# Performance work log

Measured on AMD Instinct MI355X. Metric: run time of the kernel, lower is better.

Reference implementation:

```python
import jax, jax.numpy as jnp
import numpy as np

D, H, N, BS = 3072, 2048, 16, 512
MAX_LATENT_VAR = 0.1


def setup_inputs() -> dict:
    key = jax.random.key(0)
    ks = jax.random.split(key, 12)
    s = 0.02
    return {
        "x": jax.random.normal(ks[0], (BS, D), dtype=jnp.float32),
        "eps": jax.random.normal(ks[1], (1, BS, N), dtype=jnp.float32),
        "enc_W1": jax.random.normal(ks[2], (D, H), dtype=jnp.float32) * s,
        "enc_b1": jnp.zeros((H,), dtype=jnp.float32),
        "enc_Wmu": jax.random.normal(ks[3], (H, N), dtype=jnp.float32) * s,
        "enc_bmu": jnp.zeros((N,), dtype=jnp.float32),
        "enc_Wls": jax.random.normal(ks[4], (H, 1), dtype=jnp.float32) * s,
        "enc_bls": jnp.zeros((1,), dtype=jnp.float32),
        "dec_W1": jax.random.normal(ks[5], (N, H), dtype=jnp.float32) * 0.1,
        "dec_b1": jnp.zeros((H,), dtype=jnp.float32),
        "dec_W2": jax.random.normal(ks[6], (H, D), dtype=jnp.float32) * s,
        "dec_b2": jnp.zeros((D,), dtype=jnp.float32),
    }


def reference(x, eps, enc_W1, enc_b1, enc_Wmu, enc_bmu, enc_Wls, enc_bls,
              dec_W1, dec_b1, dec_W2, dec_b2):
    bs, Dd = x.shape
    n = dec_W1.shape[0]

    def dec(z):  # smooth 2-layer MLP decoder (supports nested autodiff)
        return jnp.tanh(z @ dec_W1 + dec_b1) @ dec_W2 + dec_b2

    # encoder.forward_with_sigma
    h = jnp.tanh(x @ enc_W1 + enc_b1)
    z_star = h @ enc_Wmu + enc_bmu                      # (bs, n)
    sigma = jnp.exp(h @ enc_Wls + enc_bls)[:, 0]        # (bs,)

    # per-sample Jacobian of decoder: (bs, D, n)
    J = jax.vmap(jax.jacfwd(dec))(z_star)

    # per-sample Hessian of f(z) = stop_grad(d) . d,  d = (x - dec(z)) / sigma
    def f_hess(z, xi, sg):
        d = (xi - dec(z)) / sg
        return jnp.dot(jax.lax.stop_gradient(d), d)
    hess = jax.vmap(jax.hessian(f_hess), in_axes=(0, 0, 0))(z_star, x, sigma)  # (bs,n,n)

    eye = jnp.eye(n, dtype=x.dtype)
    Prec = jnp.einsum('bdi,bdj->bij', J, J) / (sigma ** 2)[:, None, None] + eye + hess

    eigvals = jnp.linalg.eigvalsh(Prec)                 # ascending, (bs, n)
    eigmin = eigvals[:, 0]
    delta = 1.0 / MAX_LATENT_VAR - eigmin               # (bs,)
    Prec = Prec + eye * delta[:, None, None]
    eigvals = eigvals + delta[:, None]

    # upper-triangular Cholesky: U^T U = Prec
    U = jnp.swapaxes(jnp.linalg.cholesky(Prec), -1, -2)  # (bs, n, n)

    def solve1(u, e):  # solve U y = e
        return jax.scipy.linalg.solve_triangular(u, e[:, None], lower=False)[:, 0]
    z_off = jax.vmap(jax.vmap(solve1, in_axes=(0, 0)), in_axes=(None, 0))(U, eps)  # (ne,bs,n)
    z_sample = z_star[None] + z_off

    n_eval = eps.shape[0]
    recon = dec(z_sample.reshape(-1, n)).reshape(n_eval, bs, Dd)
    recon_loss = ((recon - x[None]) ** 2).sum(axis=2).mean(axis=0) / (2.0 * sigma ** 2)
    latent_energy = (z_star ** 2).sum(axis=1) / 2.0 + (1.0 / eigvals).sum(axis=1) / 2.0
    logdet_loss = jnp.log(eigvals).sum(axis=1) / 2.0
    sigma_loss = Dd * jnp.log(sigma)
    neg_log_prob = (recon_loss + latent_energy + logdet_loss + sigma_loss) / Dd
    return (neg_log_prob, recon_loss, latent_energy, logdet_loss, sigma)
```

## Files before the change

### kernel.cpp

```cpp
#include <hip/hip_runtime.h>
#include <hip/hip_bf16.h>
#include <math.h>

#define D_ 3072
#define H_ 2048
#define N_ 16
#define BS_ 512
#define NSL_ 8

typedef short s16x8 __attribute__((ext_vector_type(8)));
typedef float f32x4v __attribute__((ext_vector_type(4)));
typedef __hip_bfloat16 bf16;

__device__ __forceinline__ void gload_lds16(const void* g, void* l) {
    __builtin_amdgcn_global_load_lds((const __attribute__((address_space(1))) void*)g,
                                     (__attribute__((address_space(3))) void*)l, 16, 0, 0);
}

__device__ __forceinline__ float bf2f(unsigned short u) {
    unsigned v = (unsigned)u << 16; float f; __builtin_memcpy(&f, &v, 4); return f;
}

__global__ __launch_bounds__(256) void mfma_nt_slab(
    const bf16* __restrict__ A, const bf16* __restrict__ Bt,
    float* __restrict__ C, int M, int N, int K, int KC)
{
    __shared__ __align__(16) bf16 As[128 * 32];
    __shared__ __align__(16) bf16 Bs[128 * 32];
    const int tid = threadIdx.x;
    const int w = tid >> 6, l = tid & 63;
    const int wr = w >> 1, wc = w & 1;
    const int m0 = blockIdx.y * 128, n0 = blockIdx.x * 128;
    const int kbeg = blockIdx.z * KC;
    float* Cz = C + (size_t)blockIdx.z * M * N;

    f32x4v acc[4][4];
    #pragma unroll
    for (int a = 0; a < 4; ++a)
        #pragma unroll
        for (int b = 0; b < 4; ++b) acc[a][b] = (f32x4v){0.f, 0.f, 0.f, 0.f};

    const int srow = l >> 2;
    const int scol = (l & 3) * 8;

    for (int k0 = kbeg; k0 < kbeg + KC; k0 += 32) {
        #pragma unroll
        for (int q = 0; q < 2; ++q) {
            int r0 = w * 32 + q * 16;
            gload_lds16(&A[(size_t)(m0 + r0 + srow) * K + k0 + scol], &As[r0 * 32]);
            gload_lds16(&Bt[(size_t)(n0 + r0 + srow) * K + k0 + scol], &Bs[r0 * 32]);
        }
        __syncthreads();
        s16x8 af[4], bfr[4];
        #pragma unroll
        for (int mf = 0; mf < 4; ++mf)
            af[mf] = *(const s16x8*)&As[(wr * 64 + mf * 16 + (l & 15)) * 32 + (l >> 4) * 8];
        #pragma unroll
        for (int nf = 0; nf < 4; ++nf)
            bfr[nf] = *(const s16x8*)&Bs[(wc * 64 + nf * 16 + (l & 15)) * 32 + (l >> 4) * 8];
        #pragma unroll
        for (int mf = 0; mf < 4; ++mf)
            #pragma unroll
            for (int nf = 0; nf < 4; ++nf)
                acc[mf][nf] = __builtin_amdgcn_mfma_f32_16x16x32_bf16(af[mf], bfr[nf], acc[mf][nf], 0, 0, 0);
        __syncthreads();
    }

    #pragma unroll
    for (int mf = 0; mf < 4; ++mf)
        #pragma unroll
        for (int nf = 0; nf < 4; ++nf) {
            int n = n0 + wc * 64 + nf * 16 + (l & 15);
            #pragma unroll
            for (int r = 0; r < 4; ++r) {
                int m = m0 + wr * 64 + mf * 16 + (l >> 4) * 4 + r;
                Cz[(size_t)m * N + n] = acc[mf][nf][r];
            }
        }
}

__global__ __launch_bounds__(256) void mfma_nt_sk(
    const bf16* __restrict__ A, const bf16* __restrict__ Bt,
    float* __restrict__ C, int M, int N, int K, int KC)
{
    __shared__ __align__(16) bf16 As[128 * 32];
    __shared__ __align__(16) bf16 Bs[128 * 32];
    const int tid = threadIdx.x;
    const int w = tid >> 6, l = tid & 63;
    const int wr = w >> 1, wc = w & 1;
    const int m0 = blockIdx.y * 128, n0 = blockIdx.x * 128;
    const int kbeg = blockIdx.z * KC;

    f32x4v acc[4][4];
    #pragma unroll
    for (int a = 0; a < 4; ++a)
        #pragma unroll
        for (int b = 0; b < 4; ++b) acc[a][b] = (f32x4v){0.f, 0.f, 0.f, 0.f};

    const int srow = l >> 2;
    const int scol = (l & 3) * 8;

    for (int k0 = kbeg; k0 < kbeg + KC; k0 += 32) {
        #pragma unroll
        for (int q = 0; q < 2; ++q) {
            int r0 = w * 32 + q * 16;
            gload_lds16(&A[(size_t)(m0 + r0 + srow) * K + k0 + scol], &As[r0 * 32]);
            gload_lds16(&Bt[(size_t)(n0 + r0 + srow) * K + k0 + scol], &Bs[r0 * 32]);
        }
        __syncthreads();
        s16x8 af[4], bfr[4];
        #pragma unroll
        for (int mf = 0; mf < 4; ++mf)
            af[mf] = *(const s16x8*)&As[(wr * 64 + mf * 16 + (l & 15)) * 32 + (l >> 4) * 8];
        #pragma unroll
        for (int nf = 0; nf < 4; ++nf)
            bfr[nf] = *(const s16x8*)&Bs[(wc * 64 + nf * 16 + (l & 15)) * 32 + (l >> 4) * 8];
        #pragma unroll
        for (int mf = 0; mf < 4; ++mf)
            #pragma unroll
            for (int nf = 0; nf < 4; ++nf)
                acc[mf][nf] = __builtin_amdgcn_mfma_f32_16x16x32_bf16(af[mf], bfr[nf], acc[mf][nf], 0, 0, 0);
        __syncthreads();
    }

    #pragma unroll
    for (int mf = 0; mf < 4; ++mf)
        #pragma unroll
        for (int nf = 0; nf < 4; ++nf) {
            int n = n0 + wc * 64 + nf * 16 + (l & 15);
            #pragma unroll
            for (int r = 0; r < 4; ++r) {
                int m = m0 + wr * 64 + mf * 16 + (l >> 4) * 4 + r;
                atomicAdd(&C[(size_t)m * N + n], acc[mf][nf][r]);
            }
        }
}

__global__ __launch_bounds__(256) void ep_ebf(const float* __restrict__ C8,
    const float* __restrict__ bias, const float* __restrict__ X,
    bf16* __restrict__ Eout, int MN, int N)
{
    const size_t SL = (size_t)MN;
    int base = (blockIdx.x * 256 + threadIdx.x) * 8;
    if (base < MN) {
        float v[8] = {0.f, 0.f, 0.f, 0.f, 0.f, 0.f, 0.f, 0.f};
        #pragma unroll
        for (int s = 0; s < NSL_; ++s) {
            float4 c0 = *(const float4*)&C8[s * SL + base];
            float4 c1 = *(const float4*)&C8[s * SL + base + 4];
            v[0] += c0.x; v[1] += c0.y; v[2] += c0.z; v[3] += c0.w;
            v[4] += c1.x; v[5] += c1.y; v[6] += c1.z; v[7] += c1.w;
        }
        float4 x0 = *(const float4*)&X[base];
        float4 x1 = *(const float4*)&X[base + 4];
        int n = base % N;
        float4 b0 = *(const float4*)&bias[n];
        float4 b1 = *(const float4*)&bias[n + 4];
        union { s16x8 vv; bf16 e[8]; } u;
        u.e[0] = __float2bfloat16(x0.x - (v[0] + b0.x));
        u.e[1] = __float2bfloat16(x0.y - (v[1] + b0.y));
        u.e[2] = __float2bfloat16(x0.z - (v[2] + b0.z));
        u.e[3] = __float2bfloat16(x0.w - (v[3] + b0.w));
        u.e[4] = __float2bfloat16(x1.x - (v[4] + b1.x));
        u.e[5] = __float2bfloat16(x1.y - (v[5] + b1.y));
        u.e[6] = __float2bfloat16(x1.z - (v[6] + b1.z));
        u.e[7] = __float2bfloat16(x1.w - (v[7] + b1.w));
        *(s16x8*)&Eout[base] = u.vv;
    }
}

__global__ __launch_bounds__(256) void ep_recon_fin(const float* __restrict__ C8,
    const float* __restrict__ bias, const float* __restrict__ X,
    const float* __restrict__ sigma, const float* __restrict__ lsig, float* __restrict__ d_out)
{
    const size_t SL = (size_t)BS_ * D_;
    int m = blockIdx.x;
    float s = 0.f;
    for (int n = threadIdx.x * 4; n < D_; n += 1024) {
        size_t i = (size_t)m * D_ + n;
        float4 acc4 = (float4){0.f, 0.f, 0.f, 0.f};
        #pragma unroll
        for (int sl = 0; sl < NSL_; ++sl) {
            float4 c = *(const float4*)&C8[sl * SL + i];
            acc4.x += c.x; acc4.y += c.y; acc4.z += c.z; acc4.w += c.w;
        }
        float4 bb = *(const float4*)&bias[n];
        float4 xx = *(const float4*)&X[i];
        float v0 = acc4.x + bb.x - xx.x;
        float v1 = acc4.y + bb.y - xx.y;
        float v2 = acc4.z + bb.z - xx.z;
        float v3 = acc4.w + bb.w - xx.w;
        s += v0 * v0 + v1 * v1 + v2 * v2 + v3 * v3;
    }
    __shared__ float red[4];
    int wid = threadIdx.x >> 6, lane = threadIdx.x & 63;
    #pragma unroll
    for (int off = 32; off; off >>= 1) s += __shfl_xor(s, off);
    if (lane == 0) red[wid] = s;
    __syncthreads();
    if (threadIdx.x == 0) {
        float tot = red[0] + red[1] + red[2] + red[3];
        float sg = sigma[m];
        float rl = tot / (2.0f * sg * sg);
        float le = d_out[2 * 512 + m];
        float ld = d_out[3 * 512 + m];
        d_out[m] = (rl + le + ld) / 3072.0f + lsig[m];
        d_out[512 + m] = rl;
    }
}

__global__ __launch_bounds__(256) void jtj_fused(
    const bf16* __restrict__ Vt, const bf16* __restrict__ W2t,
    float* __restrict__ S, int Mb, int b0)
{
    __shared__ union {
        struct { __align__(16) bf16 As[3][128 * 32]; __align__(16) bf16 Bs[3][128 * 32]; } s;
        __align__(16) bf16 J[128 * 136];
    } u;
    const int tid = threadIdx.x;
    const int w = tid >> 6, l = tid & 63;
    const int wr = w >> 1, wc = w & 1;

    int mb, nbk;
    if ((Mb & 7) == 0) {
        int lin = blockIdx.y * 24 + blockIdx.x;
        int xcd = lin & 7, idx = lin >> 3;
        int mchunk = Mb >> 3;
        mb = xcd * mchunk + idx / 24;
        nbk = idx % 24;
    } else { mb = blockIdx.y; nbk = blockIdx.x; }
    const int m0 = mb * 128, n0 = nbk * 128;

    f32x4v acc[4][4];
    #pragma unroll
    for (int a = 0; a < 4; ++a)
        #pragma unroll
        for (int b = 0; b < 4; ++b) acc[a][b] = (f32x4v){0.f, 0.f, 0.f, 0.f};

    const int strow = tid >> 2;
    const int scb = (((tid & 3) ^ ((tid >> 3) & 3)) << 4);

    auto STAGE = [&](int kt, int bi) {
        const char* a0 = (const char*)Vt  + ((size_t)(m0 + strow) * H_ + kt * 32) * 2 + scb;
        const char* b0p = (const char*)W2t + ((size_t)(n0 + strow) * H_ + kt * 32) * 2 + scb;
        char* la = (char*)u.s.As[bi] + w * 1024;
        char* lb = (char*)u.s.Bs[bi] + w * 1024;
        gload_lds16(a0, la);
        gload_lds16(a0 + (size_t)64 * H_ * 2, la + 4096);
        gload_lds16(b0p, lb);
        gload_lds16(b0p + (size_t)64 * H_ * 2, lb + 4096);
    };

    STAGE(0, 0);
    STAGE(1, 1);

    const int rdcb = (((l >> 4) ^ ((l >> 1) & 3)) << 4);

    for (int kt = 0; kt < H_ / 32; ++kt) {
        __builtin_amdgcn_sched_barrier(0);
        if (kt == H_ / 32 - 1) asm volatile("s_waitcnt vmcnt(0)" ::: "memory");
        else                   asm volatile("s_waitcnt vmcnt(4)" ::: "memory");
        __builtin_amdgcn_s_barrier();
        __builtin_amdgcn_sched_barrier(0);
        const int cur = kt % 3;
        const char* Ab = (const char*)u.s.As[cur];
        const char* Bb = (const char*)u.s.Bs[cur];
        s16x8 af[4], bfr[4];
        #pragma unroll
        for (int mf = 0; mf < 4; ++mf)
            af[mf] = *(const s16x8*)(Ab + (wr * 64 + mf * 16 + (l & 15)) * 64 + rdcb);
        #pragma unroll
        for (int nf = 0; nf < 4; ++nf)
            bfr[nf] = *(const s16x8*)(Bb + (wc * 64 + nf * 16 + (l & 15)) * 64 + rdcb);
        if (kt + 2 < H_ / 32) STAGE(kt + 2, (kt + 2) % 3);
        #pragma unroll
        for (int mf = 0; mf < 4; ++mf)
            #pragma unroll
            for (int nf = 0; nf < 4; ++nf)
                acc[mf][nf] = __builtin_amdgcn_mfma_f32_16x16x32_bf16(af[mf], bfr[nf], acc[mf][nf], 0, 0, 0);
    }

    __syncthreads();
    #pragma unroll
    for (int mf = 0; mf < 4; ++mf) {
        int rbase = wr * 64 + mf * 16 + (l >> 4) * 4;
        #pragma unroll
        for (int nf = 0; nf < 4; ++nf) {
            int col = wc * 64 + nf * 16 + (l & 15);
            #pragma unroll
            for (int r = 0; r < 4; ++r)
                u.J[(rbase + r) * 136 + col] = __float2bfloat16(acc[mf][nf][r]);
        }
    }
    __syncthreads();

    #pragma unroll
    for (int t2 = 0; t2 < 2; ++t2) {
        int bl = w * 2 + t2;
        f32x4v sp = (f32x4v){0.f, 0.f, 0.f, 0.f};
        #pragma unroll
        for (int kq = 0; kq < 4; ++kq) {
            s16x8 fr = *(const s16x8*)&u.J[(bl * 16 + (l & 15)) * 136 + kq * 32 + (l >> 4) * 8];
            sp = __builtin_amdgcn_mfma_f32_16x16x32_bf16(fr, fr, sp, 0, 0, 0);
        }
        int bglob = b0 + mb * 8 + bl;
        #pragma unroll
        for (int r = 0; r < 4; ++r)
            atomicAdd(&S[(size_t)bglob * 256 + ((l >> 4) * 4 + r) * 16 + (l & 15)], sp[r]);
    }
}

__global__ __launch_bounds__(256) void prep_all(
    const float* __restrict__ x, const float* __restrict__ enc_W1,
    const float* __restrict__ dec_W2, const float* __restrict__ dec_W1,
    bf16* __restrict__ x_bf, bf16* __restrict__ eW1t,
    bf16* __restrict__ W2t, bf16* __restrict__ W2b, bf16* __restrict__ W1b,
    float* __restrict__ zero_region)
{
    __shared__ float tile[64][65];
    const int blk = blockIdx.x;
    const int tid = threadIdx.x;
    if (blk < 768) {
        int i = blk * 256 + tid;
        const float4* p = (const float4*)x + (size_t)i * 2;
        float4 a = p[0], b = p[1];
        union { s16x8 v; bf16 e[8]; } u;
        u.e[0] = __float2bfloat16(a.x); u.e[1] = __float2bfloat16(a.y);
        u.e[2] = __float2bfloat16(a.z); u.e[3] = __float2bfloat16(a.w);
        u.e[4] = __float2bfloat16(b.x); u.e[5] = __float2bfloat16(b.y);
        u.e[6] = __float2bfloat16(b.z); u.e[7] = __float2bfloat16(b.w);
        *(s16x8*)&x_bf[(size_t)i * 8] = u.v;
    } else if (blk < 768 + 1536) {
        int bid = blk - 768;
        int r0 = (bid % 48) * 64, c0 = (bid / 48) * 64;
        int tx = tid & 63, ty = tid >> 6;
        #pragma unroll
        for (int k = 0; k < 16; ++k) {
            int rr = ty * 16 + k;
            tile[rr][tx] = enc_W1[(size_t)(r0 + rr) * H_ + c0 + tx];
        }
        __syncthreads();
        #pragma unroll
        for (int k = 0; k < 16; ++k) {
            int cc = ty * 16 + k;
            eW1t[(size_t)(c0 + cc) * D_ + r0 + tx] = __float2bfloat16(tile[tx][cc]);
        }
    } else if (blk < 768 + 3072) {
        int bid = blk - 768 - 1536;
        int r0 = (bid % 32) * 64, c0 = (bid / 32) * 64;
        int tx = tid & 63, ty = tid >> 6;
        #pragma unroll
        for (int k = 0; k < 16; ++k) {
            int rr = ty * 16 + k;
            float v = dec_W2[(size_t)(r0 + rr) * D_ + c0 + tx];
            tile[rr][tx] = v;
            W2b[(size_t)(r0 + rr) * D_ + c0 + tx] = __float2bfloat16(v);
        }
        __syncthreads();
        #pragma unroll
        for (int k = 0; k < 16; ++k) {
            int cc = ty * 16 + k;
            W2t[(size_t)(c0 + cc) * H_ + r0 + tx] = __float2bfloat16(tile[tx][cc]);
        }
    } else if (blk < 768 + 3072 + 16) {
        int i = (blk - 768 - 3072) * 256 + tid;
        if (i < N_ * H_ / 8) {
            const float4* p = (const float4*)dec_W1 + (size_t)i * 2;
            float4 a = p[0], b = p[1];
            union { s16x8 v; bf16 e[8]; } u;
            u.e[0] = __float2bfloat16(a.x); u.e[1] = __float2bfloat16(a.y);
            u.e[2] = __float2bfloat16(a.z); u.e[3] = __float2bfloat16(a.w);
            u.e[4] = __float2bfloat16(b.x); u.e[5] = __float2bfloat16(b.y);
            u.e[6] = __float2bfloat16(b.z); u.e[7] = __float2bfloat16(b.w);
            *(s16x8*)&W1b[(size_t)i * 8] = u.v;
        }
    } else {
        int i = (blk - 768 - 3072 - 16) * 256 + tid;
        *(float4*)&zero_region[(size_t)i * 4] = (float4){0.f, 0.f, 0.f, 0.f};
    }
}

__global__ __launch_bounds__(256) void zsig_t_kernel(const float* __restrict__ Ch8,
    const float* __restrict__ enc_b1, const float* __restrict__ Wmu, const float* __restrict__ bmu,
    const float* __restrict__ Wls, const float* __restrict__ bls,
    const float* __restrict__ dW1, const float* __restrict__ db1,
    float* __restrict__ z_star, float* __restrict__ lsig, float* __restrict__ sigma,
    float* __restrict__ t, bf16* __restrict__ tb, bf16* __restrict__ Vt)
{
    const int b = blockIdx.x, tid = threadIdx.x;
    const size_t SL = (size_t)BS_ * H_;
    float acc[17];
    #pragma unroll
    for (int i = 0; i < 17; ++i) acc[i] = 0.f;
    for (int hh = tid; hh < H_; hh += 256) {
        size_t idx = (size_t)b * H_ + hh;
        float c = 0.f;
        #pragma unroll
        for (int s = 0; s < NSL_; ++s) c += Ch8[s * SL + idx];
        float hv = tanhf(c + enc_b1[hh]);
        const float* wr = &Wmu[(size_t)hh * 16];
        #pragma unroll
        for (int i = 0; i < 16; ++i) acc[i] += hv * wr[i];
        acc[16] += hv * Wls[hh];
    }
    __shared__ float red[17][4];
    __shared__ float zs[16];
    __shared__ float us[H_];
    const int wid = tid >> 6, lane = tid & 63;
    #pragma unroll
    for (int i = 0; i < 17; ++i) {
        float v = acc[i];
        #pragma unroll
        for (int off = 32; off; off >>= 1) v += __shfl_xor(v, off);
        if (lane == 0) red[i][wid] = v;
    }
    __syncthreads();
    if (tid < 17) {
        float v = red[tid][0] + red[tid][1] + red[tid][2] + red[tid][3];
        if (tid < 16) { float z = v + bmu[tid]; zs[tid] = z; z_star[(size_t)b * 16 + tid] = z; }
        else { float ls = v + bls[0]; lsig[b] = ls; sigma[b] = expf(ls); }
    }
    __syncthreads();
    for (int hh = tid; hh < H_; hh += 256) {
        float a = db1[hh];
        #pragma unroll
        for (int i = 0; i < 16; ++i) a += zs[i] * dW1[(size_t)i * H_ + hh];
        float tv = tanhf(a);
        t[(size_t)b * H_ + hh] = tv;
        tb[(size_t)b * H_ + hh] = __float2bfloat16(tv);
        us[hh] = 1.f - tv * tv;
    }
    if (Vt) {
        __syncthreads();
        size_t base = (size_t)b * 16 * H_;
        int hh = tid * 8;
        for (int i = 0; i < 16; ++i) {
            union { s16x8 v; bf16 e[8]; } pk;
            #pragma unroll
            for (int k = 0; k < 8; ++k)
                pk.e[k] = __float2bfloat16(us[hh + k] * dW1[(size_t)i * H_ + hh + k]);
            *(s16x8*)&Vt[base + (size_t)i * H_ + hh] = pk.v;
        }
    }
}

__global__ __launch_bounds__(256) void build_t(const float* __restrict__ z,
    const float* __restrict__ W1, const float* __restrict__ b1, bf16* __restrict__ tb)
{
    __shared__ float zs[16];
    int b = blockIdx.x, tid = threadIdx.x;
    if (tid < 16) zs[tid] = z[(size_t)b * 16 + tid];
    __syncthreads();
    for (int hh = tid; hh < H_; hh += 256) {
        float a = b1[hh];
        #pragma unroll
        for (int i = 0; i < 16; ++i) a += zs[i] * W1[(size_t)i * H_ + hh];
        tb[(size_t)b * H_ + hh] = __float2bfloat16(tanhf(a));
    }
}

__global__ __launch_bounds__(256) void build_vt(const float* __restrict__ t,
    const float* __restrict__ W1, bf16* __restrict__ Vt, int b0)
{
    int bl = blockIdx.x, b = b0 + bl, tid = threadIdx.x;
    __shared__ float u[H_];
    for (int hh = tid; hh < H_; hh += 256) {
        float tv = t[(size_t)b * H_ + hh];
        u[hh] = 1.f - tv * tv;
    }
    __syncthreads();
    size_t base = (size_t)bl * 16 * H_;
    int hh = tid * 8;
    for (int i = 0; i < 16; ++i) {
        union { s16x8 v; bf16 e[8]; } pk;
        #pragma unroll
        for (int k = 0; k < 8; ++k)
            pk.e[k] = __float2bfloat16(u[hh + k] * W1[(size_t)i * H_ + hh + k]);
        *(s16x8*)&Vt[base + (size_t)i * H_ + hh] = pk.v;
    }
}

__global__ __launch_bounds__(256) void solve_hess_kernel(
    const float* __restrict__ S, const float* __restrict__ t, const float* __restrict__ g,
    const bf16* __restrict__ W1b, const float* __restrict__ sigma,
    const float* __restrict__ z_star, const float* __restrict__ eps,
    float* __restrict__ z_sample, float* __restrict__ d_out)
{
    __shared__ float Sh[4][256];
    const int tid = threadIdx.x;
    {
        const int w = tid >> 6, l = tid & 63;
        const int b = blockIdx.x * 4 + w;
        const int row = l & 15, kq = (l >> 4) * 8;
        f32x4v sp = (f32x4v){0.f, 0.f, 0.f, 0.f};
        for (int k0 = 0; k0 < H_; k0 += 32) {
            int kk = k0 + kq;
            s16x8 wf = *(const s16x8*)&W1b[(size_t)row * H_ + kk];
            float4 t0 = *(const float4*)&t[(size_t)b * H_ + kk];
            float4 t1 = *(const float4*)&t[(size_t)b * H_ + kk + 4];
            float4 g0 = *(const float4*)&g[(size_t)b * H_ + kk];
            float4 g1 = *(const float4*)&g[(size_t)b * H_ + kk + 4];
            float wv[8];
            wv[0] = 2.f * g0.x * t0.x * (1.f - t0.x * t0.x);
            wv[1] = 2.f * g0.y * t0.y * (1.f - t0.y * t0.y);
            wv[2] = 2.f * g0.z * t0.z * (1.f - t0.z * t0.z);
            wv[3] = 2.f * g0.w * t0.w * (1.f - t0.w * t0.w);
            wv[4] = 2.f * g1.x * t1.x * (1.f - t1.x * t1.x);
            wv[5] = 2.f * g1.y * t1.y * (1.f - t1.y * t1.y);
            wv[6] = 2.f * g1.z * t1.z * (1.f - t1.z * t1.z);
            wv[7] = 2.f * g1.w * t1.w * (1.f - t1.w * t1.w);
            union { s16x8 v; bf16 e[8]; } af;
            #pragma unroll
            for (int e = 0; e < 8; ++e)
                af.e[e] = __float2bfloat16(wv[e] * bf2f((unsigned short)wf[e]));
            sp = __builtin_amdgcn_mfma_f32_16x16x32_bf16(af.v, wf, sp, 0, 0, 0);
        }
        #pragma unroll
        for (int r = 0; r < 4; ++r)
            Sh[w][((l >> 4) * 4 + r) * 16 + (l & 15)] = sp[r];
    }
    __syncthreads();
    if (tid >= 64) return;

    const int lane = tid;
    const int q = lane >> 4;
    const int j = lane & 15;
    const int b = blockIdx.x * 4 + q;

    const float sg = sigma[b];
    const float inv_s2 = 1.0f / (sg * sg);

    float a0[16], a[16];
    #pragma unroll
    for (int r = 0; r < 16; ++r) {
        a0[r] = (S[(size_t)b * 256 + r * 16 + j] + Sh[q][r * 16 + j]) * inv_s2 + ((r == j) ? 1.0f : 0.0f);
        a[r] = a0[r];
    }

    #pragma unroll
    for (int k = 0; k < 14; ++k) {
        float x[16];
        #pragma unroll
        for (int r = 0; r < 16; ++r) x[r] = __shfl(a[k], r, 16);
        float sig2 = 0.f;
        #pragma unroll
        for (int r = 0; r < 16; ++r) if (r > k + 1) sig2 += x[r] * x[r];
        float x0 = x[k + 1];
        float normx = sqrtf(sig2 + x0 * x0);
        float alpha = (x0 >= 0.f) ? -normx : normx;
        float v[16];
        #pragma unroll
        for (int r = 0; r < 16; ++r)
            v[r] = (r <= k) ? 0.f : ((r == k + 1) ? x0 - alpha : x[r]);
        float vtv = 0.f;
        #pragma unroll
        for (int r = 0; r < 16; ++r) vtv += v[r] * v[r];
        float beta = (vtv > 1e-28f) ? 2.0f / vtv : 0.f;
        float sj = 0.f;
        #pragma unroll
        for (int r = 0; r < 16; ++r) sj += a[r] * v[r];
        float av[16];
        #pragma unroll
        for (int r = 0; r < 16; ++r) av[r] = __shfl(sj, r, 16);
        float vtav = 0.f;
        #pragma unroll
        for (int r = 0; r < 16; ++r) vtav += v[r] * av[r];
        float c = 0.5f * beta * vtav;
        float wv[16];
        #pragma unroll
        for (int r = 0; r < 16; ++r) wv[r] = beta * (av[r] - c * v[r]);
        float vj = (j <= k) ? 0.f : ((j == k + 1) ? a[k] - alpha : a[k]);
        float wj = beta * (sj - c * vj);
        #pragma unroll
        for (int r = 0; r < 16; ++r) a[r] -= v[r] * wj + wv[r] * vj;
    }

    float dg[16], eo[15];
    #pragma unroll
    for (int r = 0; r < 16; ++r) dg[r] = __shfl(a[r], r, 16);
    #pragma unroll
    for (int r = 0; r < 15; ++r) eo[r] = __shfl(a[r + 1], r, 16);

    float lo = 1e30f, hi = 1e30f;
    #pragma unroll
    for (int r = 0; r < 16; ++r) {
        float rad = ((r > 0) ? fabsf(eo[r - 1]) : 0.f) + ((r < 15) ? fabsf(eo[r]) : 0.f);
        lo = fminf(lo, dg[r] - rad);
        hi = fminf(hi, dg[r]);
    }
    lo -= 1e-4f; hi += 1e-4f;

    #pragma unroll
    for (int pass = 0; pass < 5; ++pass) {
        float step = (hi - lo) * (1.0f / 17.0f);
        float s = lo + step * (float)(j + 1);
        float qq = dg[0] - s;
        int cnt = (qq < 0.f) ? 1 : 0;
        #pragma unroll
        for (int i = 1; i < 16; ++i) {
            float denom = (fabsf(qq) < 1e-30f) ? -1e-30f : qq;
            qq = dg[i] - s - eo[i - 1] * eo[i - 1] / denom;
            cnt += (qq < 0.f) ? 1 : 0;
        }
        unsigned long long bal = __ballot(cnt >= 1);
        unsigned grp = (unsigned)((bal >> (q * 16)) & 0xffffull);
        int f = grp ? (__ffs(grp) - 1) : 16;
        float nlo = lo + step * (float)f;
        float nhi = (f < 16) ? (lo + step * (float)(f + 1)) : hi;
        lo = nlo; hi = nhi;
    }
    const float lam_min = 0.5f * (lo + hi);
    const float delta = 10.0f - lam_min;

    float bm[16];
    #pragma unroll
    for (int r = 0; r < 16; ++r) bm[r] = a0[r] + ((r == j) ? delta : 0.f);

    float ldsum = 0.f;
    #pragma unroll
    for (int kk = 0; kk < 16; ++kk) {
        float ck[16];
        #pragma unroll
        for (int r = 0; r < 16; ++r) ck[r] = __shfl(bm[kk], r, 16);
        float dkk = sqrtf(fmaxf(ck[kk], 1e-30f));
        float inv = 1.0f / dkk;
        ldsum += logf(dkk);
        float lfull[16];
        #pragma unroll
        for (int r = 0; r < 16; ++r) lfull[r] = ck[r] * inv;
        float lj = bm[kk] * inv;
        if (j == kk) {
            #pragma unroll
            for (int r = 0; r < 16; ++r) bm[r] = (r >= kk) ? lfull[r] : 0.f;
        } else if (j > kk) {
            #pragma unroll
            for (int r = 0; r < 16; ++r)
                if (r > kk) bm[r] -= lfull[r] * lj;
        }
    }

    float w[16];
    #pragma unroll
    for (int r = 0; r < 16; ++r) w[r] = 0.f;
    #pragma unroll
    for (int i = 0; i < 16; ++i) {
        float row[16];
        #pragma unroll
        for (int kx = 0; kx < 16; ++kx) row[kx] = __shfl(bm[i], kx, 16);
        float sacc = 0.f;
        #pragma unroll
        for (int kx = 0; kx < 16; ++kx) if (kx < i) sacc += row[kx] * w[kx];
        float invd = 1.0f / row[i];
        float val = (i == j) ? invd : (-sacc * invd);
        w[i] = (i >= j) ? val : 0.f;
    }

    float tsum = 0.f;
    #pragma unroll
    for (int r = 0; r < 16; ++r) tsum += w[r] * w[r];
    float zv = z_star[(size_t)b * 16 + j];
    float ep = eps[(size_t)b * 16 + j];
    float epsv[16];
    #pragma unroll
    for (int r = 0; r < 16; ++r) epsv[r] = __shfl(ep, r, 16);
    float zoff = 0.f;
    #pragma unroll
    for (int r = 0; r < 16; ++r) zoff += w[r] * epsv[r];
    z_sample[(size_t)b * 16 + j] = zv + zoff;

    float zsq = zv * zv;
    #pragma unroll
    for (int off = 1; off < 16; off <<= 1) {
        tsum += __shfl_xor(tsum, off);
        zsq  += __shfl_xor(zsq, off);
    }
    if (j == 0) {
        d_out[2 * 512 + b] = 0.5f * zsq + 0.5f * tsum;
        d_out[3 * 512 + b] = ldsum;
        d_out[4 * 512 + b] = sg;
    }
}

extern "C" void kernel_launch(void* const* d_in, const int* in_sizes, int n_in,
                              void* d_out, int out_size, void* d_ws, size_t ws_size,
                              hipStream_t stream)
{
    const float* x       = (const float*)d_in[0];
    const float* eps     = (const float*)d_in[1];
    const float* enc_W1  = (const float*)d_in[2];
    const float* enc_b1  = (const float*)d_in[3];
    const float* enc_Wmu = (const float*)d_in[4];
    const float* enc_bmu = (const float*)d_in[5];
    const float* enc_Wls = (const float*)d_in[6];
    const float* enc_bls = (const float*)d_in[7];
    const float* dec_W1  = (const float*)d_in[8];
    const float* dec_b1  = (const float*)d_in[9];
    const float* dec_W2  = (const float*)d_in[10];
    const float* dec_b2  = (const float*)d_in[11];
    float* out = (float*)d_out;

    char* wsb = (char*)d_ws;
    size_t off = 0;
    auto alloc = [&](size_t bytes) -> void* {
        off = (off + 255) & ~(size_t)255;
        void* p = wsb + off;
        off += bytes;
        return p;
    };

    float* g    = (float*)alloc((size_t)BS_ * H_ * 4);
    float* S    = (float*)alloc((size_t)BS_ * 256 * 4);

    float* Ch8  = (float*)alloc((size_t)NSL_ * BS_ * H_ * 4);
    float* Cd8  = (float*)alloc((size_t)NSL_ * BS_ * D_ * 4);
    float* t    = (float*)alloc((size_t)BS_ * H_ * 4);
    float* z_st = (float*)alloc((size_t)BS_ * 16 * 4);
    float* lsig = (float*)alloc(BS_ * 4);
    float* sigm = (float*)alloc(BS_ * 4);
    float* z_sm = (float*)alloc((size_t)BS_ * 16 * 4);
    bf16* x_bf  = (bf16*)alloc((size_t)BS_ * D_ * 2);
    bf16* eW1t  = (bf16*)alloc((size_t)H_ * D_ * 2);
    bf16* W2b   = (bf16*)alloc((size_t)H_ * D_ * 2);
    bf16* W2t   = (bf16*)alloc((size_t)D_ * H_ * 2);
    bf16* W1b   = (bf16*)alloc((size_t)N_ * H_ * 2);
    bf16* t_bf  = (bf16*)alloc((size_t)BS_ * H_ * 2);
    bf16* e_bf  = (bf16*)alloc((size_t)BS_ * D_ * 2);
    bf16* t2b   = (bf16*)alloc((size_t)BS_ * H_ * 2);

    int nb = 0;
    size_t base_off = off;
    const int cand[3] = {512, 128, 32};
    bf16* Vt = nullptr;
    for (int ci = 0; ci < 3; ++ci) {
        off = base_off;
        int n = cand[ci];
        bf16* vt = (bf16*)alloc((size_t)n * 16 * H_ * 2);
        if (off <= ws_size) { nb = n; Vt = vt; break; }
    }
    if (nb == 0) return;
    bf16* Vt_full = (nb == 512) ? Vt : nullptr;

    prep_all<<<dim3(768 + 3072 + 16 + 1152), 256, 0, stream>>>(
        x, enc_W1, dec_W2, dec_W1, x_bf, eW1t, W2t, W2b, W1b, g);

    mfma_nt_slab<<<dim3(H_ / 128, BS_ / 128, NSL_), 256, 0, stream>>>(
        x_bf, eW1t, Ch8, BS_, H_, D_, D_ / NSL_);
    zsig_t_kernel<<<dim3(BS_), 256, 0, stream>>>(Ch8, enc_b1, enc_Wmu, enc_bmu, enc_Wls, enc_bls,
        dec_W1, dec_b1, z_st, lsig, sigm, t, t_bf, Vt_full);
    mfma_nt_slab<<<dim3(D_ / 128, BS_ / 128, NSL_), 256, 0, stream>>>(
        t_bf, W2t, Cd8, BS_, D_, H_, H_ / NSL_);
    ep_ebf<<<dim3(BS_ * D_ / 8 / 256), 256, 0, stream>>>(Cd8, dec_b2, x, e_bf, BS_ * D_, D_);
    mfma_nt_sk<<<dim3(H_ / 128, BS_ / 128, 4), 256, 0, stream>>>(
        e_bf, W2b, g, BS_, H_, D_, D_ / 4);

    if (Vt_full) {
        jtj_fused<<<dim3(D_ / 128, 512 * 16 / 128), 256, 0, stream>>>(
            Vt_full, W2t, S, 512 * 16 / 128, 0);
    } else {
        for (int b0 = 0; b0 < BS_; b0 += nb) {
            build_vt<<<dim3(nb), 256, 0, stream>>>(t, dec_W1, Vt, b0);
            jtj_fused<<<dim3(D_ / 128, nb * 16 / 128), 256, 0, stream>>>(
                Vt, W2t, S, nb * 16 / 128, b0);
        }
    }

    solve_hess_kernel<<<dim3(BS_ / 4), 256, 0, stream>>>(
        S, t, g, W1b, sigm, z_st, eps, z_sm, out);
    build_t<<<dim3(BS_), 256, 0, stream>>>(z_sm, dec_W1, dec_b1, t2b);
    mfma_nt_slab<<<dim3(D_ / 128, BS_ / 128, NSL_), 256, 0, stream>>>(
        t2b, W2t, Cd8, BS_, D_, H_, H_ / NSL_);
    ep_recon_fin<<<dim3(BS_), 256, 0, stream>>>(Cd8, dec_b2, x, sigm, lsig, out);
}
```

Before: 310.6 us.

## Fuse decoder GEMM epilogue into JtJ launch and build_t into solve kernel

The first decoder GEMM (t·W2) is computed by 96 extra blocks inside the JtJ kernel launch, without split-K, writing the bf16 residual e directly. This removes the 8-slab fp32 atomic buffer, the ep_ebf reduction pass and a launch, and overlaps this GEMM with the JtJ work. The build_t step is folded into the end of solve_hess_kernel using z_sample held in shared memory, dropping another launch and a global round trip. The tradeoff is that each of the 96 e-blocks runs a full-K single-buffered loop that may become a tail, and the e_bf stores are scalar and uncoalesced.

```diff
diff --git a/kernel.cpp b/kernel.cpp
--- a/kernel.cpp
+++ b/kernel.cpp
@@ -136,39 +136,6 @@
         }
 }
 
-__global__ __launch_bounds__(256) void ep_ebf(const float* __restrict__ C8,
-    const float* __restrict__ bias, const float* __restrict__ X,
-    bf16* __restrict__ Eout, int MN, int N)
-{
-    const size_t SL = (size_t)MN;
-    int base = (blockIdx.x * 256 + threadIdx.x) * 8;
-    if (base < MN) {
-        float v[8] = {0.f, 0.f, 0.f, 0.f, 0.f, 0.f, 0.f, 0.f};
-        #pragma unroll
-        for (int s = 0; s < NSL_; ++s) {
-            float4 c0 = *(const float4*)&C8[s * SL + base];
-            float4 c1 = *(const float4*)&C8[s * SL + base + 4];
-            v[0] += c0.x; v[1] += c0.y; v[2] += c0.z; v[3] += c0.w;
-            v[4] += c1.x; v[5] += c1.y; v[6] += c1.z; v[7] += c1.w;
-        }
-        float4 x0 = *(const float4*)&X[base];
-        float4 x1 = *(const float4*)&X[base + 4];
-        int n = base % N;
-        float4 b0 = *(const float4*)&bias[n];
-        float4 b1 = *(const float4*)&bias[n + 4];
-        union { s16x8 vv; bf16 e[8]; } u;
-        u.e[0] = __float2bfloat16(x0.x - (v[0] + b0.x));
-        u.e[1] = __float2bfloat16(x0.y - (v[1] + b0.y));
-        u.e[2] = __float2bfloat16(x0.z - (v[2] + b0.z));
-        u.e[3] = __float2bfloat16(x0.w - (v[3] + b0.w));
-        u.e[4] = __float2bfloat16(x1.x - (v[4] + b1.x));
-        u.e[5] = __float2bfloat16(x1.y - (v[5] + b1.y));
-        u.e[6] = __float2bfloat16(x1.z - (v[6] + b1.z));
-        u.e[7] = __float2bfloat16(x1.w - (v[7] + b1.w));
-        *(s16x8*)&Eout[base] = u.vv;
-    }
-}
-
 __global__ __launch_bounds__(256) void ep_recon_fin(const float* __restrict__ C8,
     const float* __restrict__ bias, const float* __restrict__ X,
     const float* __restrict__ sigma, const float* __restrict__ lsig, float* __restrict__ d_out)
@@ -206,6 +173,157 @@
         float ld = d_out[3 * 512 + m];
         d_out[m] = (rl + le + ld) / 3072.0f + lsig[m];
         d_out[512 + m] = rl;
+    }
+}
+
+__global__ __launch_bounds__(256) void jtj_e_fused(
+    const bf16* __restrict__ Vt, const bf16* __restrict__ W2t,
+    float* __restrict__ S, int Mb,
+    const bf16* __restrict__ t_bf, const float* __restrict__ x,
+    const float* __restrict__ b2, bf16* __restrict__ e_bf)
+{
+    __shared__ union {
+        struct { __align__(16) bf16 As[3][128 * 32]; __align__(16) bf16 Bs[3][128 * 32]; } p;
+        __align__(16) bf16 J[128 * 136];
+        struct { __align__(16) bf16 As[128 * 32]; __align__(16) bf16 Bs[128 * 32]; } e;
+    } u;
+    const int tid = threadIdx.x;
+    const int w = tid >> 6, l = tid & 63;
+    const int wr = w >> 1, wc = w & 1;
+
+    if (blockIdx.x < 96) {
+        const int eb = blockIdx.x;
+        const int m0 = (eb / 24) * 128, n0 = (eb % 24) * 128;
+        f32x4v acc[4][4];
+        #pragma unroll
+        for (int a = 0; a < 4; ++a)
+            #pragma unroll
+            for (int b = 0; b < 4; ++b) acc[a][b] = (f32x4v){0.f, 0.f, 0.f, 0.f};
+        const int srow = l >> 2;
+        const int scol = (l & 3) * 8;
+        for (int k0 = 0; k0 < H_; k0 += 32) {
+            #pragma unroll
+            for (int q = 0; q < 2; ++q) {
+                int r0 = w * 32 + q * 16;
+                gload_lds16(&t_bf[(size_t)(m0 + r0 + srow) * H_ + k0 + scol], &u.e.As[r0 * 32]);
+                gload_lds16(&W2t[(size_t)(n0 + r0 + srow) * H_ + k0 + scol], &u.e.Bs[r0 * 32]);
+            }
+            __syncthreads();
+            s16x8 af[4], bfr[4];
+            #pragma unroll
+            for (int mf = 0; mf < 4; ++mf)
+                af[mf] = *(const s16x8*)&u.e.As[(wr * 64 + mf * 16 + (l & 15)) * 32 + (l >> 4) * 8];
+            #pragma unroll
+            for (int nf = 0; nf < 4; ++nf)
+                bfr[nf] = *(const s16x8*)&u.e.Bs[(wc * 64 + nf * 16 + (l & 15)) * 32 + (l >> 4) * 8];
+            #pragma unroll
+            for (int mf = 0; mf < 4; ++mf)
+                #pragma unroll
+                for (int nf = 0; nf < 4; ++nf)
+                    acc[mf][nf] = __builtin_amdgcn_mfma_f32_16x16x32_bf16(af[mf], bfr[nf], acc[mf][nf], 0, 0, 0);
+            __syncthreads();
+        }
+        #pragma unroll
+        for (int mf = 0; mf < 4; ++mf)
+            #pragma unroll
+            for (int nf = 0; nf < 4; ++nf) {
+                int n = n0 + wc * 64 + nf * 16 + (l & 15);
+                #pragma unroll
+                for (int r = 0; r < 4; ++r) {
+                    int m = m0 + wr * 64 + mf * 16 + (l >> 4) * 4 + r;
+                    size_t i = (size_t)m * D_ + n;
+                    e_bf[i] = __float2bfloat16(x[i] - (acc[mf][nf][r] + b2[n]));
+                }
+            }
+        return;
+    }
+
+    int lin = blockIdx.x - 96;
+    int mb, nbk;
+    if ((Mb & 7) == 0) {
+        int xcd = lin & 7, idx = lin >> 3;
+        int mchunk = Mb >> 3;
+        mb = xcd * mchunk + idx / 24;
+        nbk = idx % 24;
+    } else { mb = lin / 24; nbk = lin % 24; }
+    const int m0 = mb * 128, n0 = nbk * 128;
+
+    f32x4v acc[4][4];
+    #pragma unroll
+    for (int a = 0; a < 4; ++a)
+        #pragma unroll
+        for (int b = 0; b < 4; ++b) acc[a][b] = (f32x4v){0.f, 0.f, 0.f, 0.f};
+
+    const int strow = tid >> 2;
+    const int scb = (((tid & 3) ^ ((tid >> 3) & 3)) << 4);
+
+    auto STAGE = [&](int kt, int bi) {
+        const char* a0 = (const char*)Vt  + ((size_t)(m0 + strow) * H_ + kt * 32) * 2 + scb;
+        const char* b0p = (const char*)W2t + ((size_t)(n0 + strow) * H_ + kt * 32) * 2 + scb;
+        char* la = (char*)u.p.As[bi] + w * 1024;
+        char* lb = (char*)u.p.Bs[bi] + w * 1024;
+        gload_lds16(a0, la);
+        gload_lds16(a0 + (size_t)64 * H_ * 2, la + 4096);
+        gload_lds16(b0p, lb);
+        gload_lds16(b0p + (size_t)64 * H_ * 2, lb + 4096);
+    };
+
+    STAGE(0, 0);
+    STAGE(1, 1);
+
+    const int rdcb = (((l >> 4) ^ ((l >> 1) & 3)) << 4);
+
+    for (int kt = 0; kt < H_ / 32; ++kt) {
+        __builtin_amdgcn_sched_barrier(0);
+        if (kt == H_ / 32 - 1) asm volatile("s_waitcnt vmcnt(0)" ::: "memory");
+        else                   asm volatile("s_waitcnt vmcnt(4)" ::: "memory");
+        __builtin_amdgcn_s_barrier();
+        __builtin_amdgcn_sched_barrier(0);
+        const int cur = kt % 3;
+        const char* Ab = (const char*)u.p.As[cur];
+        const char* Bb = (const char*)u.p.Bs[cur];
+        s16x8 af[4], bfr[4];
+        #pragma unroll
+        for (int mf = 0; mf < 4; ++mf)
+            af[mf] = *(const s16x8*)(Ab + (wr * 64 + mf * 16 + (l & 15)) * 64 + rdcb);
+        #pragma unroll
+        for (int nf = 0; nf < 4; ++nf)
+            bfr[nf] = *(const s16x8*)(Bb + (wc * 64 + nf * 16 + (l & 15)) * 64 + rdcb);
+        if (kt + 2 < H_ / 32) STAGE(kt + 2, (kt + 2) % 3);
+        #pragma unroll
+        for (int mf = 0; mf < 4; ++mf)
+            #pragma unroll
+            for (int nf = 0; nf < 4; ++nf)
+                acc[mf][nf] = __builtin_amdgcn_mfma_f32_16x16x32_bf16(af[mf], bfr[nf], acc[mf][nf], 0, 0, 0);
+    }
+
+    __syncthreads();
+    #pragma unroll
+    for (int mf = 0; mf < 4; ++mf) {
+        int rbase = wr * 64 + mf * 16 + (l >> 4) * 4;
+        #pragma unroll
+        for (int nf = 0; nf < 4; ++nf) {
+            int col = wc * 64 + nf * 16 + (l & 15);
+            #pragma unroll
+            for (int r = 0; r < 4; ++r)
+                u.J[(rbase + r) * 136 + col] = __float2bfloat16(acc[mf][nf][r]);
+        }
+    }
+    __syncthreads();
+
+    #pragma unroll
+    for (int t2 = 0; t2 < 2; ++t2) {
+        int bl = w * 2 + t2;
+        f32x4v sp = (f32x4v){0.f, 0.f, 0.f, 0.f};
+        #pragma unroll
+        for (int kq = 0; kq < 4; ++kq) {
+            s16x8 fr = *(const s16x8*)&u.J[(bl * 16 + (l & 15)) * 136 + kq * 32 + (l >> 4) * 8];
+            sp = __builtin_amdgcn_mfma_f32_16x16x32_bf16(fr, fr, sp, 0, 0, 0);
+        }
+        int bglob = mb * 8 + bl;
+        #pragma unroll
+        for (int r = 0; r < 4; ++r)
+            atomicAdd(&S[(size_t)bglob * 256 + ((l >> 4) * 4 + r) * 16 + (l & 15)], sp[r]);
     }
 }
 
@@ -444,21 +562,6 @@
     }
 }
 
-__global__ __launch_bounds__(256) void build_t(const float* __restrict__ z,
-    const float* __restrict__ W1, const float* __restrict__ b1, bf16* __restrict__ tb)
-{
-    __shared__ float zs[16];
-    int b = blockIdx.x, tid = threadIdx.x;
-    if (tid < 16) zs[tid] = z[(size_t)b * 16 + tid];
-    __syncthreads();
-    for (int hh = tid; hh < H_; hh += 256) {
-        float a = b1[hh];
-        #pragma unroll
-        for (int i = 0; i < 16; ++i) a += zs[i] * W1[(size_t)i * H_ + hh];
-        tb[(size_t)b * H_ + hh] = __float2bfloat16(tanhf(a));
-    }
-}
-
 __global__ __launch_bounds__(256) void build_vt(const float* __restrict__ t,
     const float* __restrict__ W1, bf16* __restrict__ Vt, int b0)
 {
@@ -484,9 +587,11 @@
     const float* __restrict__ S, const float* __restrict__ t, const float* __restrict__ g,
     const bf16* __restrict__ W1b, const float* __restrict__ sigma,
     const float* __restrict__ z_star, const float* __restrict__ eps,
-    float* __restrict__ z_sample, float* __restrict__ d_out)
+    const float* __restrict__ dW1, const float* __restrict__ db1,
+    bf16* __restrict__ t2b, float* __restrict__ d_out)
 {
     __shared__ float Sh[4][256];
+    __shared__ float zs2[4][16];
     const int tid = threadIdx.x;
     {
         const int w = tid >> 6, l = tid & 63;
@@ -520,164 +625,177 @@
             Sh[w][((l >> 4) * 4 + r) * 16 + (l & 15)] = sp[r];
     }
     __syncthreads();
-    if (tid >= 64) return;
-
-    const int lane = tid;
-    const int q = lane >> 4;
-    const int j = lane & 15;
-    const int b = blockIdx.x * 4 + q;
-
-    const float sg = sigma[b];
-    const float inv_s2 = 1.0f / (sg * sg);
-
-    float a0[16], a[16];
-    #pragma unroll
-    for (int r = 0; r < 16; ++r) {
-        a0[r] = (S[(size_t)b * 256 + r * 16 + j] + Sh[q][r * 16 + j]) * inv_s2 + ((r == j) ? 1.0f : 0.0f);
-        a[r] = a0[r];
-    }
-
-    #pragma unroll
-    for (int k = 0; k < 14; ++k) {
-        float x[16];
-        #pragma unroll
-        for (int r = 0; r < 16; ++r) x[r] = __shfl(a[k], r, 16);
-        float sig2 = 0.f;
-        #pragma unroll
-        for (int r = 0; r < 16; ++r) if (r > k + 1) sig2 += x[r] * x[r];
-        float x0 = x[k + 1];
-        float normx = sqrtf(sig2 + x0 * x0);
-        float alpha = (x0 >= 0.f) ? -normx : normx;
-        float v[16];
-        #pragma unroll
-        for (int r = 0; r < 16; ++r)
-            v[r] = (r <= k) ? 0.f : ((r == k + 1) ? x0 - alpha : x[r]);
-        float vtv = 0.f;
-        #pragma unroll
-        for (int r = 0; r < 16; ++r) vtv += v[r] * v[r];
-        float beta = (vtv > 1e-28f) ? 2.0f / vtv : 0.f;
-        float sj = 0.f;
-        #pragma unroll
-        for (int r = 0; r < 16; ++r) sj += a[r] * v[r];
-        float av[16];
-        #pragma unroll
-        for (int r = 0; r < 16; ++r) av[r] = __shfl(sj, r, 16);
-        float vtav = 0.f;
-        #pragma unroll
-        for (int r = 0; r < 16; ++r) vtav += v[r] * av[r];
-        float c = 0.5f * beta * vtav;
-        float wv[16];
-        #pragma unroll
-        for (int r = 0; r < 16; ++r) wv[r] = beta * (av[r] - c * v[r]);
-        float vj = (j <= k) ? 0.f : ((j == k + 1) ? a[k] - alpha : a[k]);
-        float wj = beta * (sj - c * vj);
-        #pragma unroll
-        for (int r = 0; r < 16; ++r) a[r] -= v[r] * wj + wv[r] * vj;
-    }
-
-    float dg[16], eo[15];
-    #pragma unroll
-    for (int r = 0; r < 16; ++r) dg[r] = __shfl(a[r], r, 16);
-    #pragma unroll
-    for (int r = 0; r < 15; ++r) eo[r] = __shfl(a[r + 1], r, 16);
-
-    float lo = 1e30f, hi = 1e30f;
-    #pragma unroll
-    for (int r = 0; r < 16; ++r) {
-        float rad = ((r > 0) ? fabsf(eo[r - 1]) : 0.f) + ((r < 15) ? fabsf(eo[r]) : 0.f);
-        lo = fminf(lo, dg[r] - rad);
-        hi = fminf(hi, dg[r]);
-    }
-    lo -= 1e-4f; hi += 1e-4f;
-
-    #pragma unroll
-    for (int pass = 0; pass < 5; ++pass) {
-        float step = (hi - lo) * (1.0f / 17.0f);
-        float s = lo + step * (float)(j + 1);
-        float qq = dg[0] - s;
-        int cnt = (qq < 0.f) ? 1 : 0;
-        #pragma unroll
-        for (int i = 1; i < 16; ++i) {
-            float denom = (fabsf(qq) < 1e-30f) ? -1e-30f : qq;
-            qq = dg[i] - s - eo[i - 1] * eo[i - 1] / denom;
-            cnt += (qq < 0.f) ? 1 : 0;
-        }
-        unsigned long long bal = __ballot(cnt >= 1);
-        unsigned grp = (unsigned)((bal >> (q * 16)) & 0xffffull);
-        int f = grp ? (__ffs(grp) - 1) : 16;
-        float nlo = lo + step * (float)f;
-        float nhi = (f < 16) ? (lo + step * (float)(f + 1)) : hi;
-        lo = nlo; hi = nhi;
-    }
-    const float lam_min = 0.5f * (lo + hi);
-    const float delta = 10.0f - lam_min;
-
-    float bm[16];
-    #pragma unroll
-    for (int r = 0; r < 16; ++r) bm[r] = a0[r] + ((r == j) ? delta : 0.f);
-
-    float ldsum = 0.f;
-    #pragma unroll
-    for (int kk = 0; kk < 16; ++kk) {
-        float ck[16];
-        #pragma unroll
-        for (int r = 0; r < 16; ++r) ck[r] = __shfl(bm[kk], r, 16);
-        float dkk = sqrtf(fmaxf(ck[kk], 1e-30f));
-        float inv = 1.0f / dkk;
-        ldsum += logf(dkk);
-        float lfull[16];
-        #pragma unroll
-        for (int r = 0; r < 16; ++r) lfull[r] = ck[r] * inv;
-        float lj = bm[kk] * inv;
-        if (j == kk) {
-            #pragma unroll
-            for (int r = 0; r < 16; ++r) bm[r] = (r >= kk) ? lfull[r] : 0.f;
-        } else if (j > kk) {
+
+    if (tid < 64) {
+        const int lane = tid;
+        const int q = lane >> 4;
+        const int j = lane & 15;
+        const int b = blockIdx.x * 4 + q;
+
+        const float sg = sigma[b];
+        const float inv_s2 = 1.0f / (sg * sg);
+
+        float a0[16], a[16];
+        #pragma unroll
+        for (int r = 0; r < 16; ++r) {
+            a0[r] = (S[(size_t)b * 256 + r * 16 + j] + Sh[q][r * 16 + j]) * inv_s2 + ((r == j) ? 1.0f : 0.0f);
+            a[r] = a0[r];
+        }
+
+        #pragma unroll
+        for (int k = 0; k < 14; ++k) {
+            float x[16];
+            #pragma unroll
+            for (int r = 0; r < 16; ++r) x[r] = __shfl(a[k], r, 16);
+            float sig2 = 0.f;
+            #pragma unroll
+            for (int r = 0; r < 16; ++r) if (r > k + 1) sig2 += x[r] * x[r];
+            float x0 = x[k + 1];
+            float normx = sqrtf(sig2 + x0 * x0);
+            float alpha = (x0 >= 0.f) ? -normx : normx;
+            float v[16];
             #pragma unroll
             for (int r = 0; r < 16; ++r)
-                if (r > kk) bm[r] -= lfull[r] * lj;
-        }
-    }
-
-    float w[16];
-    #pragma unroll
-    for (int r = 0; r < 16; ++r) w[r] = 0.f;
-    #pragma unroll
-    for (int i = 0; i < 16; ++i) {
-        float row[16];
-        #pragma unroll
-        for (int kx = 0; kx < 16; ++kx) row[kx] = __shfl(bm[i], kx, 16);
-        float sacc = 0.f;
-        #pragma unroll
-        for (int kx = 0; kx < 16; ++kx) if (kx < i) sacc += row[kx] * w[kx];
-        float invd = 1.0f / row[i];
-        float val = (i == j) ? invd : (-sacc * invd);
-        w[i] = (i >= j) ? val : 0.f;
-    }
-
-    float tsum = 0.f;
-    #pragma unroll
-    for (int r = 0; r < 16; ++r) tsum += w[r] * w[r];
-    float zv = z_star[(size_t)b * 16 + j];
-    float ep = eps[(size_t)b * 16 + j];
-    float epsv[16];
-    #pragma unroll
-    for (int r = 0; r < 16; ++r) epsv[r] = __shfl(ep, r, 16);
-    float zoff = 0.f;
-    #pragma unroll
-    for (int r = 0; r < 16; ++r) zoff += w[r] * epsv[r];
-    z_sample[(size_t)b * 16 + j] = zv + zoff;
-
-    float zsq = zv * zv;
-    #pragma unroll
-    for (int off = 1; off < 16; off <<= 1) {
-        tsum += __shfl_xor(tsum, off);
-        zsq  += __shfl_xor(zsq, off);
-    }
-    if (j == 0) {
-        d_out[2 * 512 + b] = 0.5f * zsq + 0.5f * tsum;
-        d_out[3 * 512 + b] = ldsum;
-        d_out[4 * 512 + b] = sg;
+                v[r] = (r <= k) ? 0.f : ((r == k + 1) ? x0 - alpha : x[r]);
+            float vtv = 0.f;
+            #pragma unroll
+            for (int r = 0; r < 16; ++r) vtv += v[r] * v[r];
+            float beta = (vtv > 1e-28f) ? 2.0f / vtv : 0.f;
+            float sj = 0.f;
+            #pragma unroll
+            for (int r = 0; r < 16; ++r) sj += a[r] * v[r];
+            float av[16];
+            #pragma unroll
+            for (int r = 0; r < 16; ++r) av[r] = __shfl(sj, r, 16);
+            float vtav = 0.f;
+            #pragma unroll
+            for (int r = 0; r < 16; ++r) vtav += v[r] * av[r];
+            float c = 0.5f * beta * vtav;
+            float wv[16];
+            #pragma unroll
+            for (int r = 0; r < 16; ++r) wv[r] = beta * (av[r] - c * v[r]);
+            float vj = (j <= k) ? 0.f : ((j == k + 1) ? a[k] - alpha : a[k]);
+            float wj = beta * (sj - c * vj);
+            #pragma unroll
+            for (int r = 0; r < 16; ++r) a[r] -= v[r] * wj + wv[r] * vj;
+        }
+
+        float dg[16], eo[15];
+        #pragma unroll
+        for (int r = 0; r < 16; ++r) dg[r] = __shfl(a[r], r, 16);
+        #pragma unroll
+        for (int r = 0; r < 15; ++r) eo[r] = __shfl(a[r + 1], r, 16);
+
+        float lo = 1e30f, hi = 1e30f;
+        #pragma unroll
+        for (int r = 0; r < 16; ++r) {
+            float rad = ((r > 0) ? fabsf(eo[r - 1]) : 0.f) + ((r < 15) ? fabsf(eo[r]) : 0.f);
+            lo = fminf(lo, dg[r] - rad);
+            hi = fminf(hi, dg[r]);
+        }
+        lo -= 1e-4f; hi += 1e-4f;
+
+        #pragma unroll
+        for (int pass = 0; pass < 5; ++pass) {
+            float step = (hi - lo) * (1.0f / 17.0f);
+            float s = lo + step * (float)(j + 1);
+            float qq = dg[0] - s;
+            int cnt = (qq < 0.f) ? 1 : 0;
+            #pragma unroll
+            for (int i = 1; i < 16; ++i) {
+                float denom = (fabsf(qq) < 1e-30f) ? -1e-30f : qq;
+                qq = dg[i] - s - eo[i - 1] * eo[i - 1] / denom;
+                cnt += (qq < 0.f) ? 1 : 0;
+            }
+            unsigned long long bal = __ballot(cnt >= 1);
+            unsigned grp = (unsigned)((bal >> (q * 16)) & 0xffffull);
+            int f = grp ? (__ffs(grp) - 1) : 16;
+            float nlo = lo + step * (float)f;
+            float nhi = (f < 16) ? (lo + step * (float)(f + 1)) : hi;
+            lo = nlo; hi = nhi;
+        }
+        const float lam_min = 0.5f * (lo + hi);
+        const float delta = 10.0f - lam_min;
+
+        float bm[16];
+        #pragma unroll
+        for (int r = 0; r < 16; ++r) bm[r] = a0[r] + ((r == j) ? delta : 0.f);
+
+        float ldsum = 0.f;
+        #pragma unroll
+        for (int kk = 0; kk < 16; ++kk) {
+            float ck[16];
+            #pragma unroll
+            for (int r = 0; r < 16; ++r) ck[r] = __shfl(bm[kk], r, 16);
+            float dkk = sqrtf(fmaxf(ck[kk], 1e-30f));
+            float inv = 1.0f / dkk;
+            ldsum += logf(dkk);
+            float lfull[16];
+            #pragma unroll
+            for (int r = 0; r < 16; ++r) lfull[r] = ck[r] * inv;
+            float lj = bm[kk] * inv;
+            if (j == kk) {
+                #pragma unroll
+                for (int r = 0; r < 16; ++r) bm[r] = (r >= kk) ? lfull[r] : 0.f;
+            } else if (j > kk) {
+                #pragma unroll
+                for (int r = 0; r < 16; ++r)
+                    if (r > kk) bm[r] -= lfull[r] * lj;
+            }
+        }
+
+        float w[16];
+        #pragma unroll
+        for (int r = 0; r < 16; ++r) w[r] = 0.f;
+        #pragma unroll
+        for (int i = 0; i < 16; ++i) {
+            float row[16];
+            #pragma unroll
+            for (int kx = 0; kx < 16; ++kx) row[kx] = __shfl(bm[i], kx, 16);
+            float sacc = 0.f;
+            #pragma unroll
+            for (int kx = 0; kx < 16; ++kx) if (kx < i) sacc += row[kx] * w[kx];
+            float invd = 1.0f / row[i];
+            float val = (i == j) ? invd : (-sacc * invd);
+            w[i] = (i >= j) ? val : 0.f;
+        }
+
+        float tsum = 0.f;
+        #pragma unroll
+        for (int r = 0; r < 16; ++r) tsum += w[r] * w[r];
+        float zv = z_star[(size_t)b * 16 + j];
+        float ep = eps[(size_t)b * 16 + j];
+        float epsv[16];
+        #pragma unroll
+        for (int r = 0; r < 16; ++r) epsv[r] = __shfl(ep, r, 16);
+        float zoff = 0.f;
+        #pragma unroll
+        for (int r = 0; r < 16; ++r) zoff += w[r] * epsv[r];
+        zs2[q][j] = zv + zoff;
+
+        float zsq = zv * zv;
+        #pragma unroll
+        for (int off = 1; off < 16; off <<= 1) {
+            tsum += __shfl_xor(tsum, off);
+            zsq  += __shfl_xor(zsq, off);
+        }
+        if (j == 0) {
+            d_out[2 * 512 + b] = 0.5f * zsq + 0.5f * tsum;
+            d_out[3 * 512 + b] = ldsum;
+            d_out[4 * 512 + b] = sg;
+        }
+    }
+    __syncthreads();
+
+    {
+        const int w = tid >> 6, l = tid & 63;
+        const int b = blockIdx.x * 4 + w;
+        for (int hh = l; hh < H_; hh += 64) {
+            float a = db1[hh];
+            #pragma unroll
+            for (int i = 0; i < 16; ++i) a += zs2[w][i] * dW1[(size_t)i * H_ + hh];
+            t2b[(size_t)b * H_ + hh] = __float2bfloat16(tanhf(a));
+        }
     }
 }
 
@@ -717,7 +835,6 @@
     float* z_st = (float*)alloc((size_t)BS_ * 16 * 4);
     float* lsig = (float*)alloc(BS_ * 4);
     float* sigm = (float*)alloc(BS_ * 4);
-    float* z_sm = (float*)alloc((size_t)BS_ * 16 * 4);
     bf16* x_bf  = (bf16*)alloc((size_t)BS_ * D_ * 2);
     bf16* eW1t  = (bf16*)alloc((size_t)H_ * D_ * 2);
     bf16* W2b   = (bf16*)alloc((size_t)H_ * D_ * 2);
@@ -747,16 +864,14 @@
         x_bf, eW1t, Ch8, BS_, H_, D_, D_ / NSL_);
     zsig_t_kernel<<<dim3(BS_), 256, 0, stream>>>(Ch8, enc_b1, enc_Wmu, enc_bmu, enc_Wls, enc_bls,
         dec_W1, dec_b1, z_st, lsig, sigm, t, t_bf, Vt_full);
-    mfma_nt_slab<<<dim3(D_ / 128, BS_ / 128, NSL_), 256, 0, stream>>>(
-        t_bf, W2t, Cd8, BS_, D_, H_, H_ / NSL_);
-    ep_ebf<<<dim3(BS_ * D_ / 8 / 256), 256, 0, stream>>>(Cd8, dec_b2, x, e_bf, BS_ * D_, D_);
-    mfma_nt_sk<<<dim3(H_ / 128, BS_ / 128, 4), 256, 0, stream>>>(
-        e_bf, W2b, g, BS_, H_, D_, D_ / 4);
 
     if (Vt_full) {
-        jtj_fused<<<dim3(D_ / 128, 512 * 16 / 128), 256, 0, stream>>>(
-            Vt_full, W2t, S, 512 * 16 / 128, 0);
+        int Mb = 512 * 16 / 128;
+        jtj_e_fused<<<dim3(96 + Mb * 24), 256, 0, stream>>>(
+            Vt_full, W2t, S, Mb, t_bf, x, dec_b2, e_bf);
     } else {
+        jtj_e_fused<<<dim3(96), 256, 0, stream>>>(
+            nullptr, W2t, S, 0, t_bf, x, dec_b2, e_bf);
         for (int b0 = 0; b0 < BS_; b0 += nb) {
             build_vt<<<dim3(nb), 256, 0, stream>>>(t, dec_W1, Vt, b0);
             jtj_fused<<<dim3(D_ / 128, nb * 16 / 128), 256, 0, stream>>>(
@@ -764,9 +879,12 @@
         }
     }
 
+    mfma_nt_sk<<<dim3(H_ / 128, BS_ / 128, 4), 256, 0, stream>>>(
+        e_bf, W2b, g, BS_, H_, D_, D_ / 4);
+
     solve_hess_kernel<<<dim3(BS_ / 4), 256, 0, stream>>>(
-        S, t, g, W1b, sigm, z_st, eps, z_sm, out);
-    build_t<<<dim3(BS_), 256, 0, stream>>>(z_sm, dec_W1, dec_b1, t2b);
+        S, t, g, W1b, sigm, z_st, eps, dec_W1, dec_b1, t2b, out);
+
     mfma_nt_slab<<<dim3(D_ / 128, BS_ / 128, NSL_), 256, 0, stream>>>(
         t2b, W2t, Cd8, BS_, D_, H_, H_ / NSL_);
     ep_recon_fin<<<dim3(BS_), 256, 0, stream>>>(Cd8, dec_b2, x, sigm, lsig, out);
```

New measurement: 313.9 us. About the same (+1.1%).
